# Kernel optimization log

Measured on AMD Instinct MI355X. Metric: run time of the kernel, lower is better.

The kernel has to match this reference:

```python
import jax, jax.numpy as jnp
import numpy as np

N_NODES = 100000
N_EDGES = 600000
D = 128
BN_EPS = 1e-5


def setup_inputs() -> dict:
    key = jax.random.key(0)
    k = jax.random.split(key, 4)
    x = jax.random.normal(k[0], (N_NODES, D), dtype=jnp.float32)
    edge_index = jax.random.randint(k[1], (2, N_EDGES), 0, N_NODES, dtype=jnp.int32)
    W = jax.random.normal(k[2], (D, D), dtype=jnp.float32) * 0.05  # GCNConv weight
    b = jnp.zeros((D,), dtype=jnp.float32)                          # GCNConv bias
    gamma = jnp.ones((D,), dtype=jnp.float32)                       # BatchNorm weight
    beta = jnp.zeros((D,), dtype=jnp.float32)                       # BatchNorm bias
    return {"x": x, "edge_index": edge_index, "W": W, "b": b, "gamma": gamma, "beta": beta}


def reference(x, edge_index, W, b, gamma, beta):
    N = x.shape[0]
    # GCNConv: h = D^{-1/2} (A + I) D^{-1/2} (x W) + b
    h = x @ W  # [N, D]
    self_loops = jnp.arange(N, dtype=edge_index.dtype)
    src = jnp.concatenate([edge_index[0], self_loops])  # message source j
    dst = jnp.concatenate([edge_index[1], self_loops])  # aggregation target i
    deg = jax.ops.segment_sum(jnp.ones_like(dst, dtype=h.dtype), dst, num_segments=N)
    dinv = jax.lax.rsqrt(deg)  # deg >= 1 thanks to self-loops
    norm = dinv[src] * dinv[dst]  # [E+N]
    out = jax.ops.segment_sum(h[src] * norm[:, None], dst, num_segments=N) + b
    # BatchNorm (training-mode batch stats over nodes) + ReLU
    mean = jnp.mean(out, axis=0)
    var = jnp.mean((out - mean) ** 2, axis=0)
    out = (out - mean) * jax.lax.rsqrt(var + BN_EPS) * gamma + beta
    out = jax.nn.relu(out)
    # residual (in_ch == out_ch -> identity)
    return out + x
```

## Files before the change

kernel.cpp:

```cpp
#include <hip/hip_runtime.h>

#define NN 100000
#define NE 600000
#define DD 128
#define BN_EPS 1e-5f
#define NB1 391
#define NCV 12500
#define NFB 2344
#define NBLK 782
#define NTILES 6250

typedef __attribute__((ext_vector_type(8))) short bf16x8;
typedef __attribute__((ext_vector_type(4))) float f32x4;

static __device__ __forceinline__ unsigned short f2bf(float f) {
    unsigned u = __float_as_uint(f);
    unsigned r = (u + 0x7FFFu + ((u >> 16) & 1u)) >> 16;
    return (unsigned short)r;
}
static __device__ __forceinline__ float bflo(unsigned v) { return __uint_as_float(v << 16); }
static __device__ __forceinline__ float bfhi(unsigned v) { return __uint_as_float(v & 0xFFFF0000u); }

__global__ __launch_bounds__(256) void k_init(int* __restrict__ cnt,
                                              float* __restrict__ stats,
                                              const float* __restrict__ W,
                                              unsigned short* __restrict__ Wt) {
    int i = blockIdx.x * 256 + threadIdx.x;
    if (i < NN) cnt[i] = 0;
    if (i < 256) stats[i] = 0.0f;
    if (i < DD * DD) {
        int k = i >> 7, c = i & 127;
        Wt[c * DD + k] = f2bf(W[i]);
    }
}

__global__ __launch_bounds__(256) void k_count(const int* __restrict__ dst,
                                               int* __restrict__ cnt,
                                               int* __restrict__ rank) {
    int e = blockIdx.x * 256 + threadIdx.x;
    if (e < NE) rank[e] = atomicAdd(&cnt[dst[e]], 1);
}

__global__ __launch_bounds__(256) void k_scan1(const int* __restrict__ cnt,
                                               int* __restrict__ offs,
                                               int* __restrict__ bsum) {
    __shared__ int tmp[256];
    int tid = threadIdx.x;
    int i = blockIdx.x * 256 + tid;
    int v = (i < NN) ? (cnt[i] + 1) : 0;
    tmp[tid] = v;
    __syncthreads();
    #pragma unroll
    for (int d = 1; d < 256; d <<= 1) {
        int t = (tid >= d) ? tmp[tid - d] : 0;
        __syncthreads();
        tmp[tid] += t;
        __syncthreads();
    }
    if (i < NN) offs[i] = tmp[tid] - v;
    if (tid == 255) bsum[blockIdx.x] = tmp[255];
}

__global__ __launch_bounds__(512) void k_scan2(int* __restrict__ bsum) {
    __shared__ int tmp[512];
    int tid = threadIdx.x;
    int v = (tid < NB1) ? bsum[tid] : 0;
    tmp[tid] = v;
    __syncthreads();
    #pragma unroll
    for (int d = 1; d < 512; d <<= 1) {
        int t = (tid >= d) ? tmp[tid - d] : 0;
        __syncthreads();
        tmp[tid] += t;
        __syncthreads();
    }
    if (tid < NB1) bsum[tid] = tmp[tid] - v;
}

__global__ __launch_bounds__(256) void k_scan3(int* __restrict__ offs,
                                               const int* __restrict__ bsum,
                                               const int* __restrict__ cnt,
                                               float* __restrict__ dinv,
                                               int* __restrict__ srcs) {
    int i = blockIdx.x * 256 + threadIdx.x;
    if (i < NN) {
        int o = offs[i] + bsum[blockIdx.x];
        offs[i] = o;
        dinv[i] = rsqrtf((float)(cnt[i] + 1));
        srcs[o] = i;
        if (i == 0) offs[NN] = NE + NN;
    }
}

__global__ __launch_bounds__(256) void k_cvfill(const float* __restrict__ x,
                                                const float* __restrict__ dinv,
                                                unsigned short* __restrict__ xn,
                                                const int* __restrict__ src,
                                                const int* __restrict__ dst,
                                                const int* __restrict__ rank,
                                                const int* __restrict__ offs,
                                                int* __restrict__ srcs) {
    int bid = blockIdx.x;
    if (bid < NFB) {
        int e = bid * 256 + threadIdx.x;
        if (e < NE) {
            int t = dst[e];
            srcs[offs[t] + 1 + rank[e]] = src[e];
        }
    } else {
        int r  = (bid - NFB) * 8 + (threadIdx.x >> 5);
        int c4 = threadIdx.x & 31;
        float di = dinv[r];
        float4 v = ((const float4*)x)[(size_t)r * 32 + c4];
        unsigned p0 = ((unsigned)f2bf(v.y * di) << 16) | f2bf(v.x * di);
        unsigned p1 = ((unsigned)f2bf(v.w * di) << 16) | f2bf(v.z * di);
        ((uint2*)xn)[(size_t)r * 32 + c4] = make_uint2(p0, p1);
    }
}

__global__ __launch_bounds__(512) void k_gather(const int* __restrict__ offs,
                                                const int* __restrict__ srcs,
                                                const unsigned short* __restrict__ xn,
                                                const float* __restrict__ dinv,
                                                const float* __restrict__ b,
                                                const unsigned short* __restrict__ Wt,
                                                float* __restrict__ out,
                                                float* __restrict__ partial) {
    __shared__ uint4 Wl4[2048];
    const int tid  = threadIdx.x;
    const int wid  = tid >> 6;
    const int lane = tid & 63;
    const int lm   = lane & 15;
    const int lk   = lane >> 4;
    char* Wl = (char*)Wl4;

    #pragma unroll
    for (int it = 0; it < 4; ++it) {
        int chunk = it * 512 + tid;
        int row = chunk >> 4, c16 = chunk & 15;
        uint4 v = *(const uint4*)(Wt + row * DD + c16 * 8);
        *(uint4*)(Wl + row * 256 + ((c16 ^ (row & 7)) << 4)) = v;
    }
    float bb[8];
    #pragma unroll
    for (int nt = 0; nt < 8; ++nt) bb[nt] = b[nt * 16 + lm];
    __syncthreads();

    float s8[8], ss8[8];
    #pragma unroll
    for (int j = 0; j < 8; ++j) { s8[j] = 0.0f; ss8[j] = 0.0f; }
    const uint4* xn4 = (const uint4*)xn;

    const int tile = blockIdx.x * 8 + wid;
    if (tile < NTILES) {
        const int nbase = tile * 16;

        int   ol = offs[nbase + (lane <= 16 ? lane : 16)];
        float dv = (lane < 16) ? dinv[nbase + lane] : 0.0f;
        int   beg = __shfl(ol, lm);
        int   n   = __shfl(ol, lm + 1) - beg;
        float di  = __shfl(dv, lm);

        float acc[4][8];
        #pragma unroll
        for (int ks = 0; ks < 4; ++ks)
            #pragma unroll
            for (int j = 0; j < 8; ++j) acc[ks][j] = 0.0f;

        int k = 0;
        for (; k + 2 <= n; k += 2) {
            int s0 = srcs[beg + k];
            int s1 = srcs[beg + k + 1];
            uint4 v0[4], v1[4];
            #pragma unroll
            for (int ks = 0; ks < 4; ++ks) v0[ks] = xn4[(size_t)s0 * 16 + ks * 4 + lk];
            #pragma unroll
            for (int ks = 0; ks < 4; ++ks) v1[ks] = xn4[(size_t)s1 * 16 + ks * 4 + lk];
            #pragma unroll
            for (int ks = 0; ks < 4; ++ks) {
                acc[ks][0] += bflo(v0[ks].x) + bflo(v1[ks].x);
                acc[ks][1] += bfhi(v0[ks].x) + bfhi(v1[ks].x);
                acc[ks][2] += bflo(v0[ks].y) + bflo(v1[ks].y);
                acc[ks][3] += bfhi(v0[ks].y) + bfhi(v1[ks].y);
                acc[ks][4] += bflo(v0[ks].z) + bflo(v1[ks].z);
                acc[ks][5] += bfhi(v0[ks].z) + bfhi(v1[ks].z);
                acc[ks][6] += bflo(v0[ks].w) + bflo(v1[ks].w);
                acc[ks][7] += bfhi(v0[ks].w) + bfhi(v1[ks].w);
            }
        }
        if (k < n) {
            int s0 = srcs[beg + k];
            #pragma unroll
            for (int ks = 0; ks < 4; ++ks) {
                uint4 v = xn4[(size_t)s0 * 16 + ks * 4 + lk];
                acc[ks][0] += bflo(v.x); acc[ks][1] += bfhi(v.x);
                acc[ks][2] += bflo(v.y); acc[ks][3] += bfhi(v.y);
                acc[ks][4] += bflo(v.z); acc[ks][5] += bfhi(v.z);
                acc[ks][6] += bflo(v.w); acc[ks][7] += bfhi(v.w);
            }
        }

        bf16x8 a[4];
        #pragma unroll
        for (int ks = 0; ks < 4; ++ks)
            #pragma unroll
            for (int j = 0; j < 8; ++j) a[ks][j] = (short)f2bf(acc[ks][j] * di);

        f32x4 dacc[8];
        #pragma unroll
        for (int nt = 0; nt < 8; ++nt) dacc[nt] = (f32x4){0.f, 0.f, 0.f, 0.f};
        #pragma unroll
        for (int ks = 0; ks < 4; ++ks)
            #pragma unroll
            for (int nt = 0; nt < 8; ++nt) {
                int brow = nt * 16 + lm;
                bf16x8 bfr = *(const bf16x8*)(Wl + brow * 256 + ((ks * 64 + lk * 16) ^ ((brow & 7) << 4)));
                dacc[nt] = __builtin_amdgcn_mfma_f32_16x16x32_bf16(a[ks], bfr, dacc[nt], 0, 0, 0);
            }

        #pragma unroll
        for (int nt = 0; nt < 8; ++nt)
            #pragma unroll
            for (int r = 0; r < 4; ++r) {
                float val = dacc[nt][r] + bb[nt];
                out[(size_t)(nbase + lk * 4 + r) * DD + nt * 16 + lm] = val;
                s8[nt] += val; ss8[nt] += val * val;
            }
    }

    #pragma unroll
    for (int nt = 0; nt < 8; ++nt) {
        s8[nt]  += __shfl_xor(s8[nt], 16);  s8[nt]  += __shfl_xor(s8[nt], 32);
        ss8[nt] += __shfl_xor(ss8[nt], 16); ss8[nt] += __shfl_xor(ss8[nt], 32);
    }
    __syncthreads();
    float* sp = (float*)Wl4;
    if (lk == 0) {
        #pragma unroll
        for (int nt = 0; nt < 8; ++nt) {
            sp[wid * 128 + nt * 16 + lm]        = s8[nt];
            sp[1024 + wid * 128 + nt * 16 + lm] = ss8[nt];
        }
    }
    __syncthreads();
    if (tid < 128) {
        float a = 0.0f, c = 0.0f;
        #pragma unroll
        for (int w = 0; w < 8; ++w) { a += sp[w * 128 + tid]; c += sp[1024 + w * 128 + tid]; }
        partial[(size_t)blockIdx.x * 256 + tid]       = a;
        partial[(size_t)blockIdx.x * 256 + 128 + tid] = c;
    }
}

__global__ __launch_bounds__(256) void k_red(const float* __restrict__ partial,
                                             float* __restrict__ stats) {
    int tid = threadIdx.x;
    float a = 0.0f;
    for (int r = blockIdx.x; r < NBLK; r += 64)
        a += partial[(size_t)r * 256 + tid];
    unsafeAtomicAdd(&stats[tid], a);
}

__global__ __launch_bounds__(256) void k_final(float* __restrict__ out,
                                               const float* __restrict__ x,
                                               const float* __restrict__ gamma,
                                               const float* __restrict__ beta,
                                               const float* __restrict__ stats) {
    int idx = blockIdx.x * 256 + threadIdx.x;
    if (idx >= NN * DD / 4) return;
    int c4 = idx & 31;

    const float invN = 1.0f / (float)NN;
    float4 sm  = ((const float4*)stats)[c4];
    float4 sq  = ((const float4*)stats)[32 + c4];
    float4 g   = ((const float4*)gamma)[c4];
    float4 be  = ((const float4*)beta)[c4];
    float4 v   = ((float4*)out)[idx];
    float4 xr  = ((const float4*)x)[idx];

    float m0 = sm.x * invN, m1 = sm.y * invN, m2 = sm.z * invN, m3 = sm.w * invN;
    float r0 = rsqrtf(sq.x * invN - m0 * m0 + BN_EPS);
    float r1 = rsqrtf(sq.y * invN - m1 * m1 + BN_EPS);
    float r2 = rsqrtf(sq.z * invN - m2 * m2 + BN_EPS);
    float r3 = rsqrtf(sq.w * invN - m3 * m3 + BN_EPS);

    float4 o;
    o.x = fmaxf((v.x - m0) * r0 * g.x + be.x, 0.0f) + xr.x;
    o.y = fmaxf((v.y - m1) * r1 * g.y + be.y, 0.0f) + xr.y;
    o.z = fmaxf((v.z - m2) * r2 * g.z + be.z, 0.0f) + xr.z;
    o.w = fmaxf((v.w - m3) * r3 * g.w + be.w, 0.0f) + xr.w;
    ((float4*)out)[idx] = o;
}

extern "C" void kernel_launch(void* const* d_in, const int* in_sizes, int n_in,
                              void* d_out, int out_size, void* d_ws, size_t ws_size,
                              hipStream_t stream) {
    const float* x     = (const float*)d_in[0];
    const int*   ei    = (const int*)d_in[1];
    const float* W     = (const float*)d_in[2];
    const float* b     = (const float*)d_in[3];
    const float* gamma = (const float*)d_in[4];
    const float* beta  = (const float*)d_in[5];
    float*       out   = (float*)d_out;

    char*  base = (char*)d_ws;
    size_t off  = 0;
    auto carve = [&](size_t bytes) -> void* {
        void* p = base + off;
        off = (off + bytes + 255) & ~(size_t)255;
        return p;
    };
    unsigned short* xn    = (unsigned short*)carve((size_t)NN * DD * 2);
    float*          dinv  = (float*)carve((size_t)NN * 4);
    float*          stats = (float*)carve(256 * 4);
    int*            cnt   = (int*)carve((size_t)NN * 4);
    int*            offs  = (int*)carve((size_t)(NN + 1) * 4);
    int*            rank  = (int*)carve((size_t)NE * 4);
    int*            bsum  = (int*)carve(2048);
    int*            srcs  = (int*)carve((size_t)(NE + NN) * 4);
    unsigned short* Wt    = (unsigned short*)carve(DD * DD * 2);
    float*          partial = (float*)carve((size_t)NBLK * 256 * 4);

    const int* src = ei;
    const int* dst = ei + NE;

    k_init   <<<NB1, 256, 0, stream>>>(cnt, stats, W, Wt);
    k_count  <<<(NE + 255) / 256, 256, 0, stream>>>(dst, cnt, rank);
    k_scan1  <<<NB1, 256, 0, stream>>>(cnt, offs, bsum);
    k_scan2  <<<1, 512, 0, stream>>>(bsum);
    k_scan3  <<<NB1, 256, 0, stream>>>(offs, bsum, cnt, dinv, srcs);
    k_cvfill <<<NFB + NCV, 256, 0, stream>>>(x, dinv, xn, src, dst, rank, offs, srcs);
    k_gather <<<NBLK, 512, 0, stream>>>(offs, srcs, xn, dinv, b, Wt, out, partial);
    k_red    <<<64, 256, 0, stream>>>(partial, stats);
    k_final  <<<(NN * DD / 4 + 255) / 256, 256, 0, stream>>>(out, x, gamma, beta, stats);
}
```

Baseline: 139.0 us.

## Sort nodes by degree so gather tiles have balanced per-lane edge counts

Builds a degree histogram during the scan, prefix-sums it, and writes a permutation that groups nodes by in-degree. The gather kernel then processes 16-node tiles taken from this order, so the lanes in a wavefront loop over similar numbers of neighbors and spend less time diverged. Outputs are scattered back to the original node rows. This adds shared and global atomics in the scan kernels and makes the row writes non-contiguous, and nodes with the same degree are scattered across memory, so locality can suffer.

```diff
diff --git a/kernel.cpp b/kernel.cpp
--- a/kernel.cpp
+++ b/kernel.cpp
@@ -9,6 +9,7 @@
 #define NFB 2344
 #define NBLK 782
 #define NTILES 6250
+#define NDB 64
 
 typedef __attribute__((ext_vector_type(8))) short bf16x8;
 typedef __attribute__((ext_vector_type(4))) float f32x4;
@@ -23,11 +24,13 @@
 
 __global__ __launch_bounds__(256) void k_init(int* __restrict__ cnt,
                                               float* __restrict__ stats,
+                                              int* __restrict__ hist,
                                               const float* __restrict__ W,
                                               unsigned short* __restrict__ Wt) {
     int i = blockIdx.x * 256 + threadIdx.x;
     if (i < NN) cnt[i] = 0;
     if (i < 256) stats[i] = 0.0f;
+    if (i < NDB) hist[i] = 0;
     if (i < DD * DD) {
         int k = i >> 7, c = i & 127;
         Wt[c * DD + k] = f2bf(W[i]);
@@ -43,12 +46,15 @@
 
 __global__ __launch_bounds__(256) void k_scan1(const int* __restrict__ cnt,
                                                int* __restrict__ offs,
-                                               int* __restrict__ bsum) {
+                                               int* __restrict__ bsum,
+                                               int* __restrict__ hist) {
     __shared__ int tmp[256];
+    __shared__ int lh[NDB];
     int tid = threadIdx.x;
     int i = blockIdx.x * 256 + tid;
     int v = (i < NN) ? (cnt[i] + 1) : 0;
     tmp[tid] = v;
+    if (tid < NDB) lh[tid] = 0;
     __syncthreads();
     #pragma unroll
     for (int d = 1; d < 256; d <<= 1) {
@@ -59,13 +65,20 @@
     }
     if (i < NN) offs[i] = tmp[tid] - v;
     if (tid == 255) bsum[blockIdx.x] = tmp[255];
-}
-
-__global__ __launch_bounds__(512) void k_scan2(int* __restrict__ bsum) {
+    if (i < NN) atomicAdd(&lh[min(v - 1, NDB - 1)], 1);
+    __syncthreads();
+    if (tid < NDB && lh[tid]) atomicAdd(&hist[tid], lh[tid]);
+}
+
+__global__ __launch_bounds__(512) void k_scan2(int* __restrict__ bsum,
+                                               const int* __restrict__ hist,
+                                               int* __restrict__ gcur) {
     __shared__ int tmp[512];
+    __shared__ int h[NDB];
     int tid = threadIdx.x;
     int v = (tid < NB1) ? bsum[tid] : 0;
     tmp[tid] = v;
+    if (tid < NDB) h[tid] = hist[tid];
     __syncthreads();
     #pragma unroll
     for (int d = 1; d < 512; d <<= 1) {
@@ -75,21 +88,40 @@
         __syncthreads();
     }
     if (tid < NB1) bsum[tid] = tmp[tid] - v;
+    if (tid == 0) {
+        int run = 0;
+        for (int d = 0; d < NDB; ++d) { int c = h[d]; h[d] = run; run += c; }
+    }
+    __syncthreads();
+    if (tid < NDB) gcur[tid] = h[tid];
 }
 
 __global__ __launch_bounds__(256) void k_scan3(int* __restrict__ offs,
                                                const int* __restrict__ bsum,
                                                const int* __restrict__ cnt,
                                                float* __restrict__ dinv,
-                                               int* __restrict__ srcs) {
-    int i = blockIdx.x * 256 + threadIdx.x;
+                                               int* __restrict__ srcs,
+                                               int* __restrict__ gcur,
+                                               int* __restrict__ order) {
+    __shared__ int lh[NDB], lbase[NDB];
+    int tid = threadIdx.x;
+    int i = blockIdx.x * 256 + tid;
+    if (tid < NDB) lh[tid] = 0;
+    __syncthreads();
+    int d = 0, lrank = 0;
     if (i < NN) {
         int o = offs[i] + bsum[blockIdx.x];
         offs[i] = o;
         dinv[i] = rsqrtf((float)(cnt[i] + 1));
         srcs[o] = i;
         if (i == 0) offs[NN] = NE + NN;
-    }
+        d = min(cnt[i], NDB - 1);
+        lrank = atomicAdd(&lh[d], 1);
+    }
+    __syncthreads();
+    if (tid < NDB && lh[tid]) lbase[tid] = atomicAdd(&gcur[tid], lh[tid]);
+    __syncthreads();
+    if (i < NN) order[lbase[d] + lrank] = i;
 }
 
 __global__ __launch_bounds__(256) void k_cvfill(const float* __restrict__ x,
@@ -124,6 +156,7 @@
                                                 const float* __restrict__ dinv,
                                                 const float* __restrict__ b,
                                                 const unsigned short* __restrict__ Wt,
+                                                const int* __restrict__ order,
                                                 float* __restrict__ out,
                                                 float* __restrict__ partial) {
     __shared__ uint4 Wl4[2048];
@@ -155,11 +188,16 @@
     if (tile < NTILES) {
         const int nbase = tile * 16;
 
-        int   ol = offs[nbase + (lane <= 16 ? lane : 16)];
-        float dv = (lane < 16) ? dinv[nbase + lane] : 0.0f;
-        int   beg = __shfl(ol, lm);
-        int   n   = __shfl(ol, lm + 1) - beg;
-        float di  = __shfl(dv, lm);
+        int nodev = 0, begv = 0, nv = 0; float dvv = 0.0f;
+        if (lane < 16) {
+            nodev = order[nbase + lane];
+            int o0 = offs[nodev], o1 = offs[nodev + 1];
+            begv = o0; nv = o1 - o0;
+            dvv = dinv[nodev];
+        }
+        int   beg = __shfl(begv, lm);
+        int   n   = __shfl(nv, lm);
+        float di  = __shfl(dvv, lm);
 
         float acc[4][8];
         #pragma unroll
@@ -219,13 +257,15 @@
             }
 
         #pragma unroll
-        for (int nt = 0; nt < 8; ++nt)
-            #pragma unroll
-            for (int r = 0; r < 4; ++r) {
+        for (int r = 0; r < 4; ++r) {
+            int rnode = __shfl(nodev, lk * 4 + r);
+            #pragma unroll
+            for (int nt = 0; nt < 8; ++nt) {
                 float val = dacc[nt][r] + bb[nt];
-                out[(size_t)(nbase + lk * 4 + r) * DD + nt * 16 + lm] = val;
+                out[(size_t)rnode * DD + nt * 16 + lm] = val;
                 s8[nt] += val; ss8[nt] += val * val;
             }
+        }
     }
 
     #pragma unroll
@@ -319,18 +359,21 @@
     int*            bsum  = (int*)carve(2048);
     int*            srcs  = (int*)carve((size_t)(NE + NN) * 4);
     unsigned short* Wt    = (unsigned short*)carve(DD * DD * 2);
+    int*            hist  = (int*)carve(NDB * 4);
+    int*            gcur  = (int*)carve(NDB * 4);
+    int*            order = (int*)carve((size_t)NN * 4);
     float*          partial = (float*)carve((size_t)NBLK * 256 * 4);
 
     const int* src = ei;
     const int* dst = ei + NE;
 
-    k_init   <<<NB1, 256, 0, stream>>>(cnt, stats, W, Wt);
+    k_init   <<<NB1, 256, 0, stream>>>(cnt, stats, hist, W, Wt);
     k_count  <<<(NE + 255) / 256, 256, 0, stream>>>(dst, cnt, rank);
-    k_scan1  <<<NB1, 256, 0, stream>>>(cnt, offs, bsum);
-    k_scan2  <<<1, 512, 0, stream>>>(bsum);
-    k_scan3  <<<NB1, 256, 0, stream>>>(offs, bsum, cnt, dinv, srcs);
+    k_scan1  <<<NB1, 256, 0, stream>>>(cnt, offs, bsum, hist);
+    k_scan2  <<<1, 512, 0, stream>>>(bsum, hist, gcur);
+    k_scan3  <<<NB1, 256, 0, stream>>>(offs, bsum, cnt, dinv, srcs, gcur, order);
     k_cvfill <<<NFB + NCV, 256, 0, stream>>>(x, dinv, xn, src, dst, rank, offs, srcs);
-    k_gather <<<NBLK, 512, 0, stream>>>(offs, srcs, xn, dinv, b, Wt, out, partial);
+    k_gather <<<NBLK, 512, 0, stream>>>(offs, srcs, xn, dinv, b, Wt, order, out, partial);
     k_red    <<<64, 256, 0, stream>>>(partial, stats);
     k_final  <<<(NN * DD / 4 + 255) / 256, 256, 0, stream>>>(out, x, gamma, beta, stats);
 }
```

After: 148.8 us. 7.0% more time.
